# Kernel optimization log

Hardware: AMD Instinct MI355X
Metric: run time of the kernel (lower is better)

## Reference

```python
import jax, jax.numpy as jnp
import numpy as np

H = 16            # num heads
D = 64            # head dim
HID = 1024        # hidden size
ALPHA = 1.0       # < 2 -> power-law kernel
BANDWIDTH = 1.0
A = 0.5           # doubly-stochastic exponent
RADIUS = 1.0      # sphere radius
EPS = 1e-7


def setup_inputs() -> dict:
    key = jax.random.key(0)
    ks = jax.random.split(key, 5)
    x = jax.random.normal(ks[0], (2, 2048, HID), dtype=jnp.float32)
    s = 1.0 / np.sqrt(HID)
    qkv_w = jax.random.normal(ks[1], (3 * HID, HID), dtype=jnp.float32) * s
    qkv_b = jnp.zeros((3 * HID,), dtype=jnp.float32)
    out_w = jax.random.normal(ks[2], (HID, HID), dtype=jnp.float32) * s
    out_b = jnp.zeros((HID,), dtype=jnp.float32)
    return {"x": x, "qkv_w": qkv_w, "qkv_b": qkv_b, "out_w": out_w, "out_b": out_b}


def _l2norm(t):
    # torch F.normalize(p=2, dim=-1): divide by max(||t||, 1e-12)
    n = jnp.sqrt(jnp.sum(t * t, axis=-1, keepdims=True))
    return t / jnp.maximum(n, 1e-12)


def reference(x, qkv_w, qkv_b, out_w, out_b):
    B, S, _ = x.shape
    qkv = x @ qkv_w.T + qkv_b                       # [B,S,3*HID]
    q, k, v = jnp.split(qkv, 3, axis=-1)
    # [B,H,S,D]
    q = _l2norm(q.reshape(B, S, H, D).transpose(0, 2, 1, 3))
    k = _l2norm(k.reshape(B, S, H, D).transpose(0, 2, 1, 3))
    v = v.reshape(B, S, H, D).transpose(0, 2, 1, 3)
    # geodesic distance on the sphere
    cos = jnp.clip(jnp.einsum('bhsd,bhtd->bhst', q, k), -1.0 + EPS, 1.0 - EPS)
    g_dist = jnp.arccos(cos) * RADIUS               # [B,H,S,S]
    # alpha < 2: power-law kernel
    attn_score = (1.0 + g_dist / jnp.sqrt(BANDWIDTH)) ** (-(D + ALPHA))
    # doubly-stochastic-style rescale: diag(row^-a) @ K @ diag(col^-a)
    row = attn_score.sum(-1) ** (-A)                # [B,H,S]
    col = attn_score.sum(-2) ** (-A)                # [B,H,S]
    k_tilde = row[..., :, None] * attn_score * col[..., None, :]
    # F.normalize(p=1, dim=3): divide by max(sum |.|, 1e-12); entries >= 0
    probs = k_tilde / jnp.maximum(k_tilde.sum(-1, keepdims=True), 1e-12)
    out = jnp.einsum('bhst,bhtd->bhsd', probs, v)   # [B,H,S,D]
    out = out.transpose(0, 2, 1, 3).reshape(B, S, HID)
    return out @ out_w.T + out_b
```

## Files before the change

### kernel.cpp

```cpp
#include <hip/hip_runtime.h>
#include <math.h>

#define NH   16
#define HD   64
#define HIDN 1024
#define NB   2
#define SEQ  2048
#define ROWS (NB*SEQ)
#define BH   (NB*NH)

typedef __attribute__((ext_vector_type(8))) short bf16x8;
typedef __attribute__((ext_vector_type(8))) _Float16 f16x8;
typedef __attribute__((ext_vector_type(4))) float f32x4;
typedef _Float16 f16;

__device__ __forceinline__ unsigned short f2bf(float f) {
    unsigned u = __float_as_uint(f);
    u += 0x7FFF + ((u >> 16) & 1);
    return (unsigned short)(u >> 16);
}
__device__ __forceinline__ bf16x8 ldfrag(const unsigned short* p) {
    return *(const bf16x8*)p;
}
__device__ __forceinline__ f16x8 ldfragh(const f16* p) {
    return *(const f16x8*)p;
}
__device__ __forceinline__ f32x4 mfma16(bf16x8 a, bf16x8 b, f32x4 c) {
    return __builtin_amdgcn_mfma_f32_16x16x32_bf16(a, b, c, 0, 0, 0);
}
__device__ __forceinline__ f32x4 mfma16h(f16x8 a, f16x8 b, f32x4 c) {
    return __builtin_amdgcn_mfma_f32_16x16x32_f16(a, b, c, 0, 0, 0);
}

__device__ __forceinline__ float log2_1pacos(float c) {
    float u = fmaxf(1.0f - c, 0.0f);
    float s = __builtin_amdgcn_sqrtf(u);
    float p = fmaf(u, 2.68532e-3f, 7.89259e-3f);
    p = fmaf(u, p, 2.6516504e-2f);
    p = fmaf(u, p, 1.1785113e-1f);
    p = fmaf(u, p, 1.4142136f);
    return __builtin_amdgcn_logf(fmaf(s, p, 1.0f));
}

__global__ __launch_bounds__(256)
void conv_f16(const float* __restrict__ src, f16* __restrict__ dst) {
    int i = (blockIdx.x * 256 + threadIdx.x) * 8;
    float4 a = *(const float4*)(src + i);
    float4 b = *(const float4*)(src + i + 4);
    f16x8 o = { (f16)a.x, (f16)a.y, (f16)a.z, (f16)a.w,
                (f16)b.x, (f16)b.y, (f16)b.z, (f16)b.w };
    *(f16x8*)(dst + i) = o;
}

__global__ __launch_bounds__(256)
void gemm_nt_f16(const f16* __restrict__ A, const f16* __restrict__ B,
                 const float* __restrict__ bias, float* __restrict__ C,
                 int M, int N, int K)
{
    __shared__ f16 As[128 * 32];
    __shared__ f16 Bs[128 * 32];
    const int tid = threadIdx.x;
    const int lane = tid & 63, w = tid >> 6;
    const int ln = lane & 15, lq = lane >> 4;
    const int wm = (w >> 1) * 64, wn = (w & 1) * 64;
    const int m0 = blockIdx.x * 128, n0 = blockIdx.y * 128;

    const int srow = tid >> 1;
    const int scol = (tid & 1) * 16;
    const f16* Ag = A + (size_t)(m0 + srow) * K + scol;
    const f16* Bg = B + (size_t)(n0 + srow) * K + scol;
    f16* Asw = As + srow * 32 + scol;
    f16* Bsw = Bs + srow * 32 + scol;

    f32x4 acc[4][4];
    #pragma unroll
    for (int i = 0; i < 4; ++i)
        #pragma unroll
        for (int j = 0; j < 4; ++j) acc[i][j] = (f32x4){0.f, 0.f, 0.f, 0.f};

    for (int kc = 0; kc < K; kc += 32) {
        uint4 a0 = *(const uint4*)(Ag + kc);
        uint4 a1 = *(const uint4*)(Ag + kc + 8);
        uint4 b0 = *(const uint4*)(Bg + kc);
        uint4 b1 = *(const uint4*)(Bg + kc + 8);
        __syncthreads();
        *(uint4*)Asw = a0; *(uint4*)(Asw + 8) = a1;
        *(uint4*)Bsw = b0; *(uint4*)(Bsw + 8) = b1;
        __syncthreads();
        f16x8 af[4], bf[4];
        #pragma unroll
        for (int i = 0; i < 4; ++i)
            af[i] = *(const f16x8*)&As[(wm + i * 16 + ln) * 32 + lq * 8];
        #pragma unroll
        for (int j = 0; j < 4; ++j)
            bf[j] = *(const f16x8*)&Bs[(wn + j * 16 + ln) * 32 + lq * 8];
        #pragma unroll
        for (int i = 0; i < 4; ++i)
            #pragma unroll
            for (int j = 0; j < 4; ++j)
                acc[i][j] = mfma16h(af[i], bf[j], acc[i][j]);
    }

    #pragma unroll
    for (int i = 0; i < 4; ++i) {
        #pragma unroll
        for (int j = 0; j < 4; ++j) {
            int colIdx = n0 + wn + j * 16 + ln;
            float bs = bias[colIdx];
            #pragma unroll
            for (int r = 0; r < 4; ++r) {
                int row = m0 + wm + i * 16 + lq * 4 + r;
                C[(size_t)row * N + colIdx] = acc[i][j][r] + bs;
            }
        }
    }
}

__global__ __launch_bounds__(256)
void normalize_qk_f16(const float* __restrict__ qkv,
                      f16* __restrict__ qf, f16* __restrict__ kf)
{
    int w    = blockIdx.x * 4 + (threadIdx.x >> 6);
    int lane = threadIdx.x & 63;
    int n = w >> 4, h = w & 15;
    int b = n >> 11, s = n & 2047;
    const float* base = qkv + (size_t)n * 3 * HIDN + h * HD;
    float q = base[lane], k = base[HIDN + lane];
    float qs = q * q, ks = k * k;
    #pragma unroll
    for (int o = 32; o; o >>= 1) { qs += __shfl_xor(qs, o); ks += __shfl_xor(ks, o); }
    q *= 1.0f / fmaxf(sqrtf(qs), 1e-12f);
    k *= 1.0f / fmaxf(sqrtf(ks), 1e-12f);
    size_t idx = ((size_t)((b * NH + h) * SEQ + s)) * HD + lane;
    qf[idx] = (f16)q;
    kf[idx] = (f16)k;
}

__global__ __launch_bounds__(256)
void v_transpose(const float* __restrict__ qkv, unsigned short* __restrict__ vth)
{
    __shared__ float Ls[64][65];
    int bh = blockIdx.y, s0 = blockIdx.x * 64;
    int b = bh >> 4, h = bh & 15;
    int tid = threadIdx.x;
    #pragma unroll
    for (int i = 0; i < 4; ++i) {
        int idx = tid + i * 256;
        int row = idx >> 4, c4 = (idx & 15) * 4;
        float4 v = *(const float4*)&qkv[((size_t)(b * SEQ + s0 + row)) * 3 * HIDN
                                        + 2 * HIDN + h * HD + c4];
        Ls[row][c4+0] = v.x; Ls[row][c4+1] = v.y; Ls[row][c4+2] = v.z; Ls[row][c4+3] = v.w;
    }
    __syncthreads();
    int d = tid >> 2, sb = (tid & 3) * 16;
    unsigned short hi[16];
    #pragma unroll
    for (int j = 0; j < 16; ++j) hi[j] = f2bf(Ls[sb + j][d]);
    size_t o = ((size_t)bh * HD + d) * SEQ + s0 + sb;
    *(uint4*)&vth[o]     = *(uint4*)&hi[0];
    *(uint4*)&vth[o + 8] = *(uint4*)&hi[8];
}

#define KSTR 72

__global__ __launch_bounds__(256)
void col_sum_f16(const f16* __restrict__ qf, const f16* __restrict__ kf,
                 float* __restrict__ colp)
{
    __shared__ __align__(16) f16 Qs[64 * KSTR];
    int bh = blockIdx.y, z = blockIdx.z;
    int tid = threadIdx.x, w = tid >> 6, lane = tid & 63, ln = lane & 15, lq = lane >> 4;
    int m0 = blockIdx.x * 64 + w * 16;
    int s_base = z * (SEQ / 2);
    const f16* qb = qf + (size_t)bh * SEQ * HD;
    const int sr = tid >> 3;
    const int sc = (tid & 7) * 8;

    size_t rowK = ((size_t)bh * SEQ + m0 + ln) * HD;
    f16x8 kf0 = ldfragh(kf + rowK + lq * 8), kf1 = ldfragh(kf + rowK + 32 + lq * 8);

    uint4 qa = *(const uint4*)(qb + (size_t)(s_base + sr) * HD + sc);
    uint4 qc = *(const uint4*)(qb + (size_t)(s_base + sr + 32) * HD + sc);

    float cacc[4] = {0.f, 0.f, 0.f, 0.f};
    #pragma unroll 1
    for (int st = 0; st < SEQ / 128; ++st) {
        __syncthreads();
        *(uint4*)&Qs[sr * KSTR + sc] = qa;
        *(uint4*)&Qs[(sr + 32) * KSTR + sc] = qc;
        int sn = s_base + ((st + 1 < SEQ / 128) ? (st + 1) * 64 : 0);
        qa = *(const uint4*)(qb + (size_t)(sn + sr) * HD + sc);
        qc = *(const uint4*)(qb + (size_t)(sn + sr + 32) * HD + sc);
        __syncthreads();
        #pragma unroll
        for (int nt = 0; nt < 4; ++nt) {
            const f16* qp = &Qs[(nt * 16 + ln) * KSTR + lq * 8];
            f32x4 sacc = {0.f, 0.f, 0.f, 0.f};
            sacc = mfma16h(kf0, *(const f16x8*)qp, sacc);
            sacc = mfma16h(kf1, *(const f16x8*)(qp + 32), sacc);
            #pragma unroll
            for (int r = 0; r < 4; ++r)
                cacc[r] += __builtin_amdgcn_exp2f(-65.0f * log2_1pacos(sacc[r]));
        }
    }
    #pragma unroll
    for (int r = 0; r < 4; ++r) {
        float v = cacc[r];
        v += __shfl_xor(v, 1); v += __shfl_xor(v, 2);
        v += __shfl_xor(v, 4); v += __shfl_xor(v, 8);
        if (ln == 0)
            colp[((size_t)z * BH + bh) * SEQ + m0 + lq * 4 + r] = v;
    }
}

__global__ __launch_bounds__(256)
void col_finalize(const float* __restrict__ colp, float* __restrict__ col)
{
    int i = (blockIdx.x * 256 + threadIdx.x) * 4;
    float4 a = *(const float4*)&colp[i];
    float4 b = *(const float4*)&colp[(size_t)BH * SEQ + i];
    float4 o;
    o.x = -0.5f * __builtin_amdgcn_logf(a.x + b.x);
    o.y = -0.5f * __builtin_amdgcn_logf(a.y + b.y);
    o.z = -0.5f * __builtin_amdgcn_logf(a.z + b.z);
    o.w = -0.5f * __builtin_amdgcn_logf(a.w + b.w);
    *(float4*)&col[i] = o;
}

__global__ __launch_bounds__(256)
void attn_f16(const f16* __restrict__ qf, const f16* __restrict__ kf,
              const unsigned short* __restrict__ vth,
              const float* __restrict__ col,
              float* __restrict__ nump, float* __restrict__ denp)
{
    __shared__ __align__(16) f16 Ks[64 * KSTR];
    __shared__ __align__(16) unsigned short Vs[64 * KSTR];
    __shared__ __align__(16) unsigned short Ws[4][16 * KSTR];
    __shared__ float lcls[64];
    int bh = blockIdx.y, z = blockIdx.z;
    int tid = threadIdx.x, w = tid >> 6, lane = tid & 63, ln = lane & 15, lq = lane >> 4;
    int m0 = blockIdx.x * 64 + w * 16;
    int t_base = z * (SEQ / 2);
    unsigned short* ws = Ws[w];

    const f16* kb = kf + (size_t)bh * SEQ * HD;
    const unsigned short* vb = vth + (size_t)bh * HD * SEQ;
    const float* cb = col + (size_t)bh * SEQ;

    const int sr = tid >> 3;
    const int sc = (tid & 7) * 8;

    size_t rowQ = ((size_t)bh * SEQ + m0 + ln) * HD;
    f16x8 qf0 = ldfragh(qf + rowQ + lq * 8), qf1 = ldfragh(qf + rowQ + 32 + lq * 8);

    bf16x8 ones;
    #pragma unroll
    for (int i = 0; i < 8; ++i) ones[i] = (short)0x3F80;

    f32x4 num[4];
    #pragma unroll
    for (int nt = 0; nt < 4; ++nt) num[nt] = (f32x4){0.f, 0.f, 0.f, 0.f};
    f32x4 den = {0.f, 0.f, 0.f, 0.f};

    uint4 ka = *(const uint4*)(kb + (size_t)(t_base + sr) * HD + sc);
    uint4 kc = *(const uint4*)(kb + (size_t)(t_base + sr + 32) * HD + sc);
    uint4 va = *(const uint4*)(vb + (size_t)sr * SEQ + t_base + sc);
    uint4 vc = *(const uint4*)(vb + (size_t)(sr + 32) * SEQ + t_base + sc);
    float clv = (tid < 64) ? cb[t_base + tid] : 0.f;

    #pragma unroll 1
    for (int tt = 0; tt < SEQ / 128; ++tt) {
        __syncthreads();
        *(uint4*)&Ks[sr * KSTR + sc] = ka;
        *(uint4*)&Ks[(sr + 32) * KSTR + sc] = kc;
        *(uint4*)&Vs[sr * KSTR + sc] = va;
        *(uint4*)&Vs[(sr + 32) * KSTR + sc] = vc;
        if (tid < 64) lcls[tid] = clv;
        int tn = t_base + ((tt + 1 < SEQ / 128) ? (tt + 1) * 64 : 0);
        ka = *(const uint4*)(kb + (size_t)(tn + sr) * HD + sc);
        kc = *(const uint4*)(kb + (size_t)(tn + sr + 32) * HD + sc);
        va = *(const uint4*)(vb + (size_t)sr * SEQ + tn + sc);
        vc = *(const uint4*)(vb + (size_t)(sr + 32) * SEQ + tn + sc);
        clv = (tid < 64) ? cb[tn + tid] : 0.f;
        __syncthreads();

        #pragma unroll
        for (int nt = 0; nt < 4; ++nt) {
            const f16* kp = &Ks[(nt * 16 + ln) * KSTR + lq * 8];
            f32x4 sacc = {0.f, 0.f, 0.f, 0.f};
            sacc = mfma16h(qf0, *(const f16x8*)kp, sacc);
            sacc = mfma16h(qf1, *(const f16x8*)(kp + 32), sacc);
            float lcl = lcls[nt * 16 + ln];
            #pragma unroll
            for (int r = 0; r < 4; ++r) {
                float l = log2_1pacos(sacc[r]);
                float wv = __builtin_amdgcn_exp2f(fmaf(l, -65.0f, lcl));
                ws[(lq * 4 + r) * KSTR + nt * 16 + ln] =
                    (unsigned short)(__float_as_uint(wv) >> 16);
            }
        }
        bf16x8 wa0 = ldfrag(ws + ln * KSTR + lq * 8);
        bf16x8 wa1 = ldfrag(ws + ln * KSTR + 32 + lq * 8);
        den = mfma16(wa0, ones, den);
        den = mfma16(wa1, ones, den);
        #pragma unroll
        for (int nt = 0; nt < 4; ++nt) {
            const unsigned short* vp = &Vs[(nt * 16 + ln) * KSTR + lq * 8];
            num[nt] = mfma16(wa0, *(const bf16x8*)vp, num[nt]);
            num[nt] = mfma16(wa1, *(const bf16x8*)(vp + 32), num[nt]);
        }
    }

    if (ln == 0) {
        #pragma unroll
        for (int r = 0; r < 4; ++r)
            denp[((size_t)z * BH + bh) * SEQ + m0 + lq * 4 + r] = den[r];
    }
    float* np = nump + (((size_t)z * BH + bh) * (SEQ / 64) + blockIdx.x) * 4096
                + (size_t)(w * 16) * 64;
    #pragma unroll
    for (int nt = 0; nt < 4; ++nt)
        #pragma unroll
        for (int r = 0; r < 4; ++r)
            np[(lq * 4 + r) * 64 + nt * 16 + ln] = num[nt][r];
}

__global__ __launch_bounds__(256)
void attn_combine(const float* __restrict__ nump, const float* __restrict__ denp,
                  f16* __restrict__ ctx)
{
    int sT = blockIdx.x, bh = blockIdx.y;
    int b = bh >> 4, h = bh & 15;
    int tid = threadIdx.x;
    int s_l = tid >> 2, dg = (tid & 3) * 16;
    const float* p0 = nump + (((size_t)bh) * (SEQ / 64) + sT) * 4096 + s_l * 64 + dg;
    const float* p1 = nump + (((size_t)BH + bh) * (SEQ / 64) + sT) * 4096 + s_l * 64 + dg;
    int s = sT * 64 + s_l;
    float den = denp[(size_t)bh * SEQ + s] + denp[((size_t)BH + bh) * SEQ + s];
    float inv = 1.0f / fmaxf(den, 1e-12f);
    f16 o[16];
    #pragma unroll
    for (int j4 = 0; j4 < 4; ++j4) {
        float4 a = *(const float4*)(p0 + j4 * 4);
        float4 c = *(const float4*)(p1 + j4 * 4);
        o[j4*4+0] = (f16)((a.x + c.x) * inv);
        o[j4*4+1] = (f16)((a.y + c.y) * inv);
        o[j4*4+2] = (f16)((a.z + c.z) * inv);
        o[j4*4+3] = (f16)((a.w + c.w) * inv);
    }
    f16* dst = ctx + ((size_t)(b * SEQ + s)) * HIDN + h * HD + dg;
    *(f16x8*)dst = *(f16x8*)&o[0];
    *(f16x8*)(dst + 8) = *(f16x8*)&o[8];
}

extern "C" void kernel_launch(void* const* d_in, const int* in_sizes, int n_in,
                              void* d_out, int out_size, void* d_ws, size_t ws_size,
                              hipStream_t stream) {
    const float* x      = (const float*)d_in[0];
    const float* qkv_w  = (const float*)d_in[1];
    const float* qkv_b  = (const float*)d_in[2];
    const float* out_w  = (const float*)d_in[3];
    const float* out_b  = (const float*)d_in[4];
    float* out = (float*)d_out;

    const size_t NTT = (size_t)BH * SEQ * HD;
    float* qkv = (float*)d_ws;
    float* nump = qkv;
    float* denp = nump + (size_t)2 * BH * (SEQ/64) * 4096;
    float* colp = denp + (size_t)2 * BH * SEQ;
    float* col = qkv + (size_t)ROWS * 3 * HIDN;
    f16* xh    = (f16*)(col + (size_t)BH * SEQ);
    f16* wqh   = xh + (size_t)ROWS * HIDN;
    f16* woh   = wqh + (size_t)3 * HIDN * HIDN;
    f16* ctxh  = woh + (size_t)HIDN * HIDN;
    f16* qfp   = ctxh + (size_t)ROWS * HIDN;
    f16* kfp   = qfp + NTT;
    unsigned short* vth = (unsigned short*)(kfp + NTT);

    conv_f16<<<ROWS*HIDN/2048, 256, 0, stream>>>(x, xh);
    conv_f16<<<3*HIDN*HIDN/2048, 256, 0, stream>>>(qkv_w, wqh);
    conv_f16<<<HIDN*HIDN/2048, 256, 0, stream>>>(out_w, woh);

    gemm_nt_f16<<<dim3(ROWS/128, 3*HIDN/128), 256, 0, stream>>>(
        xh, wqh, qkv_b, qkv, ROWS, 3*HIDN, HIDN);
    normalize_qk_f16<<<ROWS*NH/4, 256, 0, stream>>>(qkv, qfp, kfp);
    v_transpose<<<dim3(SEQ/64, BH), 256, 0, stream>>>(qkv, vth);
    col_sum_f16<<<dim3(SEQ/64, BH, 2), 256, 0, stream>>>(qfp, kfp, colp);
    col_finalize<<<BH*SEQ/1024, 256, 0, stream>>>(colp, col);
    attn_f16<<<dim3(SEQ/64, BH, 2), 256, 0, stream>>>(qfp, kfp, vth, col, nump, denp);
    attn_combine<<<dim3(SEQ/64, BH), 256, 0, stream>>>(nump, denp, ctxh);
    gemm_nt_f16<<<dim3(ROWS/128, HIDN/128), 256, 0, stream>>>(
        ctxh, woh, out_b, out, ROWS, HIDN, HIDN);
}
```

Before: 332.0 us.

## Drop split-K in attention and col-sum, load GEMM tiles via global_load_lds

Removes the two-way split over the key dimension in col_sum and attention, so each block walks the full sequence and writes normalized ctx directly. This eliminates the attn_combine kernel and the partial numerator/denominator buffers. Separately, the GEMM stages its A/B tiles with direct global-to-LDS loads instead of going through registers. The trade-off is half as many blocks (1024 instead of 2048) for the attention kernels, which lowers occupancy and parallelism.

```diff
diff --git a/kernel.cpp b/kernel.cpp
--- a/kernel.cpp
+++ b/kernel.cpp
@@ -13,6 +13,12 @@
 typedef __attribute__((ext_vector_type(8))) _Float16 f16x8;
 typedef __attribute__((ext_vector_type(4))) float f32x4;
 typedef _Float16 f16;
+
+typedef const __attribute__((address_space(1))) void GV;
+typedef __attribute__((address_space(3))) void LV;
+__device__ __forceinline__ void glds16(const void* g, void* l) {
+    __builtin_amdgcn_global_load_lds((GV*)g, (LV*)l, 16, 0, 0);
+}
 
 __device__ __forceinline__ unsigned short f2bf(float f) {
     unsigned u = __float_as_uint(f);
@@ -65,12 +71,12 @@
     const int wm = (w >> 1) * 64, wn = (w & 1) * 64;
     const int m0 = blockIdx.x * 128, n0 = blockIdx.y * 128;
 
-    const int srow = tid >> 1;
-    const int scol = (tid & 1) * 16;
-    const f16* Ag = A + (size_t)(m0 + srow) * K + scol;
-    const f16* Bg = B + (size_t)(n0 + srow) * K + scol;
-    f16* Asw = As + srow * 32 + scol;
-    f16* Bsw = Bs + srow * 32 + scol;
+    const int grow = lane >> 2;
+    const int gcol = (lane & 3) * 8;
+    const f16* Ab = A + (size_t)(m0 + w * 32 + grow) * K + gcol;
+    const f16* Bb = B + (size_t)(n0 + w * 32 + grow) * K + gcol;
+    f16* Asw = As + (w * 32) * 32;
+    f16* Bsw = Bs + (w * 32) * 32;
 
     f32x4 acc[4][4];
     #pragma unroll
@@ -79,13 +85,12 @@
         for (int j = 0; j < 4; ++j) acc[i][j] = (f32x4){0.f, 0.f, 0.f, 0.f};
 
     for (int kc = 0; kc < K; kc += 32) {
-        uint4 a0 = *(const uint4*)(Ag + kc);
-        uint4 a1 = *(const uint4*)(Ag + kc + 8);
-        uint4 b0 = *(const uint4*)(Bg + kc);
-        uint4 b1 = *(const uint4*)(Bg + kc + 8);
-        __syncthreads();
-        *(uint4*)Asw = a0; *(uint4*)(Asw + 8) = a1;
-        *(uint4*)Bsw = b0; *(uint4*)(Bsw + 8) = b1;
+        __syncthreads();
+        #pragma unroll
+        for (int i = 0; i < 2; ++i) {
+            glds16(Ab + (size_t)(i * 16) * K + kc, Asw + (i * 16) * 32);
+            glds16(Bb + (size_t)(i * 16) * K + kc, Bsw + (i * 16) * 32);
+        }
         __syncthreads();
         f16x8 af[4], bf[4];
         #pragma unroll
@@ -168,10 +173,9 @@
                  float* __restrict__ colp)
 {
     __shared__ __align__(16) f16 Qs[64 * KSTR];
-    int bh = blockIdx.y, z = blockIdx.z;
+    int bh = blockIdx.y;
     int tid = threadIdx.x, w = tid >> 6, lane = tid & 63, ln = lane & 15, lq = lane >> 4;
     int m0 = blockIdx.x * 64 + w * 16;
-    int s_base = z * (SEQ / 2);
     const f16* qb = qf + (size_t)bh * SEQ * HD;
     const int sr = tid >> 3;
     const int sc = (tid & 7) * 8;
@@ -179,16 +183,16 @@
     size_t rowK = ((size_t)bh * SEQ + m0 + ln) * HD;
     f16x8 kf0 = ldfragh(kf + rowK + lq * 8), kf1 = ldfragh(kf + rowK + 32 + lq * 8);
 
-    uint4 qa = *(const uint4*)(qb + (size_t)(s_base + sr) * HD + sc);
-    uint4 qc = *(const uint4*)(qb + (size_t)(s_base + sr + 32) * HD + sc);
+    uint4 qa = *(const uint4*)(qb + (size_t)sr * HD + sc);
+    uint4 qc = *(const uint4*)(qb + (size_t)(sr + 32) * HD + sc);
 
     float cacc[4] = {0.f, 0.f, 0.f, 0.f};
     #pragma unroll 1
-    for (int st = 0; st < SEQ / 128; ++st) {
+    for (int st = 0; st < SEQ / 64; ++st) {
         __syncthreads();
         *(uint4*)&Qs[sr * KSTR + sc] = qa;
         *(uint4*)&Qs[(sr + 32) * KSTR + sc] = qc;
-        int sn = s_base + ((st + 1 < SEQ / 128) ? (st + 1) * 64 : 0);
+        int sn = (st + 1 < SEQ / 64) ? (st + 1) * 64 : 0;
         qa = *(const uint4*)(qb + (size_t)(sn + sr) * HD + sc);
         qc = *(const uint4*)(qb + (size_t)(sn + sr + 32) * HD + sc);
         __syncthreads();
@@ -209,7 +213,7 @@
         v += __shfl_xor(v, 1); v += __shfl_xor(v, 2);
         v += __shfl_xor(v, 4); v += __shfl_xor(v, 8);
         if (ln == 0)
-            colp[((size_t)z * BH + bh) * SEQ + m0 + lq * 4 + r] = v;
+            colp[(size_t)bh * SEQ + m0 + lq * 4 + r] = v;
     }
 }
 
@@ -218,29 +222,27 @@
 {
     int i = (blockIdx.x * 256 + threadIdx.x) * 4;
     float4 a = *(const float4*)&colp[i];
-    float4 b = *(const float4*)&colp[(size_t)BH * SEQ + i];
     float4 o;
-    o.x = -0.5f * __builtin_amdgcn_logf(a.x + b.x);
-    o.y = -0.5f * __builtin_amdgcn_logf(a.y + b.y);
-    o.z = -0.5f * __builtin_amdgcn_logf(a.z + b.z);
-    o.w = -0.5f * __builtin_amdgcn_logf(a.w + b.w);
+    o.x = -0.5f * __builtin_amdgcn_logf(a.x);
+    o.y = -0.5f * __builtin_amdgcn_logf(a.y);
+    o.z = -0.5f * __builtin_amdgcn_logf(a.z);
+    o.w = -0.5f * __builtin_amdgcn_logf(a.w);
     *(float4*)&col[i] = o;
 }
 
 __global__ __launch_bounds__(256)
 void attn_f16(const f16* __restrict__ qf, const f16* __restrict__ kf,
               const unsigned short* __restrict__ vth,
-              const float* __restrict__ col,
-              float* __restrict__ nump, float* __restrict__ denp)
+              const float* __restrict__ col, f16* __restrict__ ctx)
 {
     __shared__ __align__(16) f16 Ks[64 * KSTR];
     __shared__ __align__(16) unsigned short Vs[64 * KSTR];
     __shared__ __align__(16) unsigned short Ws[4][16 * KSTR];
     __shared__ float lcls[64];
-    int bh = blockIdx.y, z = blockIdx.z;
+    int bh = blockIdx.y;
+    int b = bh >> 4, h = bh & 15;
     int tid = threadIdx.x, w = tid >> 6, lane = tid & 63, ln = lane & 15, lq = lane >> 4;
     int m0 = blockIdx.x * 64 + w * 16;
-    int t_base = z * (SEQ / 2);
     unsigned short* ws = Ws[w];
 
     const f16* kb = kf + (size_t)bh * SEQ * HD;
@@ -262,21 +264,22 @@
     for (int nt = 0; nt < 4; ++nt) num[nt] = (f32x4){0.f, 0.f, 0.f, 0.f};
     f32x4 den = {0.f, 0.f, 0.f, 0.f};
 
-    uint4 ka = *(const uint4*)(kb + (size_t)(t_base + sr) * HD + sc);
-    uint4 kc = *(const uint4*)(kb + (size_t)(t_base + sr + 32) * HD + sc);
-    uint4 va = *(const uint4*)(vb + (size_t)sr * SEQ + t_base + sc);
-    uint4 vc = *(const uint4*)(vb + (size_t)(sr + 32) * SEQ + t_base + sc);
-    float clv = (tid < 64) ? cb[t_base + tid] : 0.f;
+    uint4 ka = *(const uint4*)(kb + (size_t)sr * HD + sc);
+    uint4 kc = *(const uint4*)(kb + (size_t)(sr + 32) * HD + sc);
+    uint4 va = *(const uint4*)(vb + (size_t)sr * SEQ + sc);
+    uint4 vc = *(const uint4*)(vb + (size_t)(sr + 32) * SEQ + sc);
+    float clv = (tid < 64) ? cb[tid] : 0.f;
 
     #pragma unroll 1
-    for (int tt = 0; tt < SEQ / 128; ++tt) {
+    for (int tt = 0; tt < SEQ / 64; ++tt) {
+        int t0 = tt * 64;
         __syncthreads();
         *(uint4*)&Ks[sr * KSTR + sc] = ka;
         *(uint4*)&Ks[(sr + 32) * KSTR + sc] = kc;
         *(uint4*)&Vs[sr * KSTR + sc] = va;
         *(uint4*)&Vs[(sr + 32) * KSTR + sc] = vc;
         if (tid < 64) lcls[tid] = clv;
-        int tn = t_base + ((tt + 1 < SEQ / 128) ? (tt + 1) * 64 : 0);
+        int tn = (tt + 1 < SEQ / 64) ? (tt + 1) * 64 : 0;
         ka = *(const uint4*)(kb + (size_t)(tn + sr) * HD + sc);
         kc = *(const uint4*)(kb + (size_t)(tn + sr + 32) * HD + sc);
         va = *(const uint4*)(vb + (size_t)sr * SEQ + tn + sc);
@@ -311,46 +314,15 @@
         }
     }
 
-    if (ln == 0) {
-        #pragma unroll
-        for (int r = 0; r < 4; ++r)
-            denp[((size_t)z * BH + bh) * SEQ + m0 + lq * 4 + r] = den[r];
-    }
-    float* np = nump + (((size_t)z * BH + bh) * (SEQ / 64) + blockIdx.x) * 4096
-                + (size_t)(w * 16) * 64;
-    #pragma unroll
-    for (int nt = 0; nt < 4; ++nt)
-        #pragma unroll
-        for (int r = 0; r < 4; ++r)
-            np[(lq * 4 + r) * 64 + nt * 16 + ln] = num[nt][r];
-}
-
-__global__ __launch_bounds__(256)
-void attn_combine(const float* __restrict__ nump, const float* __restrict__ denp,
-                  f16* __restrict__ ctx)
-{
-    int sT = blockIdx.x, bh = blockIdx.y;
-    int b = bh >> 4, h = bh & 15;
-    int tid = threadIdx.x;
-    int s_l = tid >> 2, dg = (tid & 3) * 16;
-    const float* p0 = nump + (((size_t)bh) * (SEQ / 64) + sT) * 4096 + s_l * 64 + dg;
-    const float* p1 = nump + (((size_t)BH + bh) * (SEQ / 64) + sT) * 4096 + s_l * 64 + dg;
-    int s = sT * 64 + s_l;
-    float den = denp[(size_t)bh * SEQ + s] + denp[((size_t)BH + bh) * SEQ + s];
-    float inv = 1.0f / fmaxf(den, 1e-12f);
-    f16 o[16];
-    #pragma unroll
-    for (int j4 = 0; j4 < 4; ++j4) {
-        float4 a = *(const float4*)(p0 + j4 * 4);
-        float4 c = *(const float4*)(p1 + j4 * 4);
-        o[j4*4+0] = (f16)((a.x + c.x) * inv);
-        o[j4*4+1] = (f16)((a.y + c.y) * inv);
-        o[j4*4+2] = (f16)((a.z + c.z) * inv);
-        o[j4*4+3] = (f16)((a.w + c.w) * inv);
-    }
-    f16* dst = ctx + ((size_t)(b * SEQ + s)) * HIDN + h * HD + dg;
-    *(f16x8*)dst = *(f16x8*)&o[0];
-    *(f16x8*)(dst + 8) = *(f16x8*)&o[8];
+    #pragma unroll
+    for (int r = 0; r < 4; ++r) {
+        float inv = 1.0f / fmaxf(den[r], 1e-12f);
+        int s = m0 + lq * 4 + r;
+        #pragma unroll
+        for (int nt = 0; nt < 4; ++nt)
+            ctx[((size_t)(b * SEQ + s)) * HIDN + h * HD + nt * 16 + ln] =
+                (f16)(num[nt][r] * inv);
+    }
 }
 
 extern "C" void kernel_launch(void* const* d_in, const int* in_sizes, int n_in,
@@ -365,9 +337,7 @@
 
     const size_t NTT = (size_t)BH * SEQ * HD;
     float* qkv = (float*)d_ws;
-    float* nump = qkv;
-    float* denp = nump + (size_t)2 * BH * (SEQ/64) * 4096;
-    float* colp = denp + (size_t)2 * BH * SEQ;
+    float* colp = qkv;
     float* col = qkv + (size_t)ROWS * 3 * HIDN;
     f16* xh    = (f16*)(col + (size_t)BH * SEQ);
     f16* wqh   = xh + (size_t)ROWS * HIDN;
@@ -385,10 +355,9 @@
         xh, wqh, qkv_b, qkv, ROWS, 3*HIDN, HIDN);
     normalize_qk_f16<<<ROWS*NH/4, 256, 0, stream>>>(qkv, qfp, kfp);
     v_transpose<<<dim3(SEQ/64, BH), 256, 0, stream>>>(qkv, vth);
-    col_sum_f16<<<dim3(SEQ/64, BH, 2), 256, 0, stream>>>(qfp, kfp, colp);
+    col_sum_f16<<<dim3(SEQ/64, BH), 256, 0, stream>>>(qfp, kfp, colp);
     col_finalize<<<BH*SEQ/1024, 256, 0, stream>>>(colp, col);
-    attn_f16<<<dim3(SEQ/64, BH, 2), 256, 0, stream>>>(qfp, kfp, vth, col, nump, denp);
-    attn_combine<<<dim3(SEQ/64, BH), 256, 0, stream>>>(nump, denp, ctxh);
+    attn_f16<<<dim3(SEQ/64, BH), 256, 0, stream>>>(qfp, kfp, vth, col, ctxh);
     gemm_nt_f16<<<dim3(ROWS/128, HIDN/128), 256, 0, stream>>>(
         ctxh, woh, out_b, out, ROWS, HIDN, HIDN);
 }
```

After: 328.0 us. Within noise of the previous version (-1.2%).
